# Kernel tuning notes

Measured on AMD Instinct MI355X. Metric: run time of the kernel, lower is better.

The kernel has to match this reference:

```python
import jax, jax.numpy as jnp
import numpy as np

N = 50000      # nodes
E = 640000     # edges
D = 128        # input/hidden dim
L = 3          # GIN layers
G = 256        # graphs in batch
LAT = 64       # latent dim
BN_EPS = 1e-5
SLOPE = 0.2    # LeakyReLU negative slope


def _leaky(h):
    return jnp.where(h >= 0, h, SLOPE * h)


def setup_inputs() -> dict:
    key = jax.random.key(0)
    ks = jax.random.split(key, 8)
    x = jax.random.normal(ks[0], (N, D), dtype=jnp.float32)
    edge_index = jax.random.randint(ks[1], (2, E), 0, N, dtype=jnp.int64)
    batch = jnp.sort(jax.random.randint(ks[2], (N,), 0, G, dtype=jnp.int64))
    W1 = jax.random.normal(ks[3], (L, D, D), dtype=jnp.float32) * 0.05
    W2 = jax.random.normal(ks[4], (L, D, D), dtype=jnp.float32) * 0.05
    fc_W = jax.random.normal(ks[5], (LAT, D), dtype=jnp.float32) * 0.05
    return {
        "x": x,
        "W1": W1,
        "b1": jnp.zeros((L, D), jnp.float32),
        "bn_g": jnp.ones((L, D), jnp.float32),
        "bn_b": jnp.zeros((L, D), jnp.float32),
        "bn_m": jnp.zeros((L, D), jnp.float32),
        "bn_v": jax.random.uniform(ks[6], (L, D), jnp.float32, 0.5, 1.5),
        "W2": W2,
        "b2": jnp.zeros((L, D), jnp.float32),
        "out_g": jnp.ones((D,), jnp.float32),
        "out_b": jnp.zeros((D,), jnp.float32),
        "out_m": jnp.zeros((D,), jnp.float32),
        "out_v": jax.random.uniform(ks[7], (D,), jnp.float32, 0.5, 1.5),
        "fc_W": fc_W,
        "fc_b": jnp.zeros((LAT,), jnp.float32),
        "edge_index": edge_index,
        "batch": batch,
    }


def reference(x, W1, b1, bn_g, bn_b, bn_m, bn_v, W2, b2,
              out_g, out_b, out_m, out_v, fc_W, fc_b,
              edge_index, batch):
    src, dst = edge_index[0], edge_index[1]
    for i in range(L):
        # GINConv: (1+eps)*x + sum_{j in N(i)} x_j  (eps=0 default)
        agg = x + jax.ops.segment_sum(x[src], dst, num_segments=N)
        # MLP: Linear -> LeakyReLU -> BatchNorm(eval) -> Linear -> LeakyReLU
        h = _leaky(agg @ W1[i].T + b1[i])
        h = (h - bn_m[i]) * jax.lax.rsqrt(bn_v[i] + BN_EPS) * bn_g[i] + bn_b[i]
        x = _leaky(h @ W2[i].T + b2[i])
        # dropout is identity in eval mode
    pooled = jax.ops.segment_sum(x, batch, num_segments=G)  # [G, D]
    out = (pooled - out_m) * jax.lax.rsqrt(out_v + BN_EPS) * out_g + out_b
    return out @ fc_W.T + fc_b  # [G, LAT]
```

## Files before the change

kernel.cpp:

```cpp
#include <hip/hip_runtime.h>
#include <cstdint>
#include <cstddef>

#define NN 50000
#define EE 640000
#define DD 128
#define LL 3
#define GG 256
#define LATD 64

typedef __attribute__((ext_vector_type(8))) __bf16 bf16x8;
typedef __attribute__((ext_vector_type(4))) float f32x4;

__device__ __forceinline__ unsigned short f2bf(float f) {
  __bf16 h = (__bf16)f;
  return __builtin_bit_cast(unsigned short, h);
}
__device__ __forceinline__ float bf2f(unsigned int u16) {
  unsigned int x = u16 << 16;
  return __builtin_bit_cast(float, x);
}
__device__ __forceinline__ void unpack8(uint4 v, float* f) {
  f[0] = bf2f(v.x & 0xffffu); f[1] = bf2f(v.x >> 16);
  f[2] = bf2f(v.y & 0xffffu); f[3] = bf2f(v.y >> 16);
  f[4] = bf2f(v.z & 0xffffu); f[5] = bf2f(v.z >> 16);
  f[6] = bf2f(v.w & 0xffffu); f[7] = bf2f(v.w >> 16);
}
__device__ __forceinline__ void acc8(uint4 v, float* f) {
  f[0] += bf2f(v.x & 0xffffu); f[1] += bf2f(v.x >> 16);
  f[2] += bf2f(v.y & 0xffffu); f[3] += bf2f(v.y >> 16);
  f[4] += bf2f(v.z & 0xffffu); f[5] += bf2f(v.z >> 16);
  f[6] += bf2f(v.w & 0xffffu); f[7] += bf2f(v.w >> 16);
}
__device__ __forceinline__ uint4 pack8(const float* f) {
  uint4 v;
  v.x = f2bf(f[0]) | ((unsigned)f2bf(f[1]) << 16);
  v.y = f2bf(f[2]) | ((unsigned)f2bf(f[3]) << 16);
  v.z = f2bf(f[4]) | ((unsigned)f2bf(f[5]) << 16);
  v.w = f2bf(f[6]) | ((unsigned)f2bf(f[7]) << 16);
  return v;
}

#define SWZ(byte_, row_) ((byte_) ^ (((row_) & 7) << 4))
#define CPAD 4

#define CVT_BLK 3125
#define WCV_BLK 48
#define HIST_BLK 2500
__global__ __launch_bounds__(256) void prep_kernel(
    const float4* __restrict__ x, uint4* __restrict__ xb,
    const float* __restrict__ W1, const float* __restrict__ W2,
    uint4* __restrict__ wb, const int* __restrict__ dst,
    int* __restrict__ counts) {
  int b = blockIdx.x;
  if (b < CVT_BLK) {
    int t = b * 256 + threadIdx.x;
    float4 a = x[t * 2], bb = x[t * 2 + 1];
    float f[8] = {a.x, a.y, a.z, a.w, bb.x, bb.y, bb.z, bb.w};
    xb[t] = pack8(f);
  } else if (b < CVT_BLK + WCV_BLK) {
    int t = (b - CVT_BLK) * 256 + threadIdx.x;
    int m = t >> 11;
    int q = t & 2047;
    int byte = q * 16;
    int row = byte >> 8;
    int inner = byte & 255;
    int isrc = inner ^ ((row & 7) << 4);
    int k0 = isrc >> 1;
    const float* Wsrc = (m & 1) ? W2 : W1;
    const float* p = Wsrc + ((size_t)(m >> 1) * DD * DD + row * DD + k0);
    float4 f0 = ((const float4*)p)[0], f1 = ((const float4*)p)[1];
    float f[8] = {f0.x, f0.y, f0.z, f0.w, f1.x, f1.y, f1.z, f1.w};
    wb[(size_t)m * 2048 + q] = pack8(f);
  } else {
    int e = (b - CVT_BLK - WCV_BLK) * 256 + threadIdx.x;
    atomicAdd(&counts[dst[e] << CPAD], 1);
  }
}

__global__ __launch_bounds__(256) void scan1_kernel(const int* __restrict__ counts,
                                                    int* __restrict__ rp,
                                                    int* __restrict__ bsum, int n) {
  int i = blockIdx.x * 256 + threadIdx.x;
  int v = (i < n) ? counts[i << CPAD] : 0;
  int lane = threadIdx.x & 63, w = threadIdx.x >> 6;
  int s = v;
#pragma unroll
  for (int off = 1; off < 64; off <<= 1) {
    int u = __shfl_up(s, off);
    if (lane >= off) s += u;
  }
  __shared__ int ws[4];
  if (lane == 63) ws[w] = s;
  __syncthreads();
  int add = 0;
#pragma unroll
  for (int k = 0; k < 4; ++k) if (k < w) add += ws[k];
  int incl = s + add;
  if (i < n) rp[i] = incl - v;
  if (threadIdx.x == 255) bsum[blockIdx.x] = incl;
}

__global__ __launch_bounds__(256) void scan2_kernel(int* __restrict__ bsum, int nb) {
  int t = threadIdx.x;
  int v = (t < nb) ? bsum[t] : 0;
  int lane = t & 63, w = t >> 6;
  int s = v;
#pragma unroll
  for (int off = 1; off < 64; off <<= 1) {
    int u = __shfl_up(s, off);
    if (lane >= off) s += u;
  }
  __shared__ int ws[4];
  if (lane == 63) ws[w] = s;
  __syncthreads();
  int add = 0;
#pragma unroll
  for (int k = 0; k < 4; ++k) if (k < w) add += ws[k];
  int incl = s + add;
  if (t < nb) bsum[t] = incl - v;
}

__global__ __launch_bounds__(256) void scan3_kernel(int* __restrict__ rp,
                                                    int* __restrict__ cursor,
                                                    const int* __restrict__ bsum, int n) {
  int i = blockIdx.x * 256 + threadIdx.x;
  if (i < n) {
    int v = rp[i] + bsum[blockIdx.x];
    rp[i] = v;
    cursor[i << CPAD] = v;
  }
  if (i == 0) rp[n] = EE;
}

__global__ __launch_bounds__(256) void fill_kernel(const int* __restrict__ src,
                                                   const int* __restrict__ dst,
                                                   int* __restrict__ cursor,
                                                   int* __restrict__ col, int E) {
  int e = blockIdx.x * blockDim.x + threadIdx.x;
  if (e < E) {
    int p = atomicAdd(&cursor[dst[e] << CPAD], 1);
    col[p] = src[e];
  }
}

__global__ __launch_bounds__(256, 4) void agg_kernel(const uint4* __restrict__ xin,
                                                     const int* __restrict__ row_ptr,
                                                     const int* __restrict__ colv,
                                                     uint4* __restrict__ agg, int n) {
  int tid = blockIdx.x * 256 + threadIdx.x;
  int node = tid >> 4;
  int c = tid & 15;
  if (node >= n) return;
  float acc[8];
  unpack8(xin[(size_t)node * 16 + c], acc);
  int s = row_ptr[node], e = row_ptr[node + 1];
  int j = s;
  for (; j + 8 <= e; j += 8) {
    int i0 = colv[j],     i1 = colv[j + 1], i2 = colv[j + 2], i3 = colv[j + 3];
    int i4 = colv[j + 4], i5 = colv[j + 5], i6 = colv[j + 6], i7 = colv[j + 7];
    uint4 v0 = xin[(size_t)i0 * 16 + c];
    uint4 v1 = xin[(size_t)i1 * 16 + c];
    uint4 v2 = xin[(size_t)i2 * 16 + c];
    uint4 v3 = xin[(size_t)i3 * 16 + c];
    uint4 v4 = xin[(size_t)i4 * 16 + c];
    uint4 v5 = xin[(size_t)i5 * 16 + c];
    uint4 v6 = xin[(size_t)i6 * 16 + c];
    uint4 v7 = xin[(size_t)i7 * 16 + c];
    acc8(v0, acc); acc8(v1, acc); acc8(v2, acc); acc8(v3, acc);
    acc8(v4, acc); acc8(v5, acc); acc8(v6, acc); acc8(v7, acc);
  }
  for (; j + 2 <= e; j += 2) {
    uint4 v0 = xin[(size_t)colv[j] * 16 + c];
    uint4 v1 = xin[(size_t)colv[j + 1] * 16 + c];
    acc8(v0, acc); acc8(v1, acc);
  }
  if (j < e) acc8(xin[(size_t)colv[j] * 16 + c], acc);
  agg[(size_t)node * 16 + c] = pack8(acc);
}

__global__ __launch_bounds__(512) void mlp128(
    const uint4* __restrict__ aggb, unsigned short* __restrict__ xout,
    const uint4* __restrict__ w1b, const uint4* __restrict__ w2b,
    const float* __restrict__ b1, const float* __restrict__ bng,
    const float* __restrict__ bnb, const float* __restrict__ bnm,
    const float* __restrict__ bnv, const float* __restrict__ b2, int n) {
  __shared__ __align__(16) char smem[98304];
  char* w1p = smem;
  char* w2p = smem + 32768;
  char* xp  = smem + 65536;

#pragma unroll
  for (int it = 0; it < 8; ++it) {
    int q = it * 512 + threadIdx.x;
    ((uint4*)w1p)[q] = w1b[q];
    ((uint4*)w2p)[q] = w2b[q];
  }

  int lane = threadIdx.x & 63;
  int c = lane & 15;
  int kq = lane >> 4;
  int wave = threadIdx.x >> 6;
  int r0 = wave * 16;

  float b1v[8], sv[8], tv[8], b2v[8];
#pragma unroll
  for (int ni = 0; ni < 8; ++ni) {
    int cc = ni * 16 + c;
    b1v[ni] = b1[cc];
    float s = bng[cc] * rsqrtf(bnv[cc] + 1e-5f);
    sv[ni] = s;
    tv[ni] = bnb[cc] - bnm[cc] * s;
    b2v[ni] = b2[cc];
  }

  for (int tile = blockIdx.x; tile * 128 < n; tile += 256) {
    int base = tile * 128;
#pragma unroll
    for (int it = 0; it < 4; ++it) {
      int t = it * 512 + threadIdx.x;
      int row = t >> 4, cc = t & 15;
      int grow = base + row;
      uint4 v = make_uint4(0, 0, 0, 0);
      if (grow < n) v = aggb[(size_t)grow * 16 + cc];
      *(uint4*)(xp + SWZ(row * 256 + cc * 16, row)) = v;
    }
    __syncthreads();

    f32x4 acc[8];
#pragma unroll
    for (int ni = 0; ni < 8; ++ni) acc[ni] = (f32x4){0.f, 0.f, 0.f, 0.f};

#pragma unroll
    for (int ks = 0; ks < 4; ++ks) {
      int row = r0 + c;
      bf16x8 a = *(const bf16x8*)(xp + SWZ(row * 256 + ks * 64 + kq * 16, row));
#pragma unroll
      for (int ni = 0; ni < 8; ++ni) {
        int wr = ni * 16 + c;
        bf16x8 bfr = *(const bf16x8*)(w1p + SWZ(wr * 256 + ks * 64 + kq * 16, wr));
        acc[ni] = __builtin_amdgcn_mfma_f32_16x16x32_bf16(a, bfr, acc[ni], 0, 0, 0);
      }
    }

#pragma unroll
    for (int ni = 0; ni < 8; ++ni)
#pragma unroll
      for (int r = 0; r < 4; ++r) {
        float h = acc[ni][r] + b1v[ni];
        h = h >= 0.f ? h : 0.2f * h;
        h = h * sv[ni] + tv[ni];
        int row = r0 + kq * 4 + r;
        *(__bf16*)(xp + SWZ(row * 256 + (ni * 16 + c) * 2, row)) = (__bf16)h;
      }
    __syncthreads();

#pragma unroll
    for (int ni = 0; ni < 8; ++ni) acc[ni] = (f32x4){0.f, 0.f, 0.f, 0.f};

#pragma unroll
    for (int ks = 0; ks < 4; ++ks) {
      int row = r0 + c;
      bf16x8 a = *(const bf16x8*)(xp + SWZ(row * 256 + ks * 64 + kq * 16, row));
#pragma unroll
      for (int ni = 0; ni < 8; ++ni) {
        int wr = ni * 16 + c;
        bf16x8 bfr = *(const bf16x8*)(w2p + SWZ(wr * 256 + ks * 64 + kq * 16, wr));
        acc[ni] = __builtin_amdgcn_mfma_f32_16x16x32_bf16(a, bfr, acc[ni], 0, 0, 0);
      }
    }

#pragma unroll
    for (int ni = 0; ni < 8; ++ni)
#pragma unroll
      for (int r = 0; r < 4; ++r) {
        float xo = acc[ni][r] + b2v[ni];
        xo = xo >= 0.f ? xo : 0.2f * xo;
        int grow = base + r0 + kq * 4 + r;
        if (grow < n) xout[(size_t)grow * DD + ni * 16 + c] = f2bf(xo);
      }
    __syncthreads();
  }
}

__global__ __launch_bounds__(256) void pool_kernel(const uint4* __restrict__ x,
                                                   const int* __restrict__ batch,
                                                   float* __restrict__ pooled, int n) {
  int gid = blockIdx.x * 256 + threadIdx.x;
  int grp = gid >> 4, c = gid & 15;
  int n0 = grp * 16;
  if (n0 >= n) return;
  float acc[8] = {0.f, 0.f, 0.f, 0.f, 0.f, 0.f, 0.f, 0.f};
  int curg = batch[n0];
  int end = n0 + 16 < n ? n0 + 16 : n;
  for (int node = n0; node < end; ++node) {
    int g = batch[node];
    if (g != curg) {
      float* p = pooled + (size_t)curg * DD + c * 8;
#pragma unroll
      for (int i = 0; i < 8; ++i) { atomicAdd(p + i, acc[i]); acc[i] = 0.f; }
      curg = g;
    }
    float tmp[8];
    unpack8(x[(size_t)node * 16 + c], tmp);
#pragma unroll
    for (int i = 0; i < 8; ++i) acc[i] += tmp[i];
  }
  float* p = pooled + (size_t)curg * DD + c * 8;
#pragma unroll
  for (int i = 0; i < 8; ++i) atomicAdd(p + i, acc[i]);
}

__global__ __launch_bounds__(128) void head_kernel(const float* __restrict__ pooled,
    const float* __restrict__ og, const float* __restrict__ ob,
    const float* __restrict__ om, const float* __restrict__ ov,
    const float* __restrict__ fcW, const float* __restrict__ fcb,
    float* __restrict__ out) {
  __shared__ float pb[DD];
  int g = blockIdx.x;
  int t = threadIdx.x;
  float s = og[t] * rsqrtf(ov[t] + 1e-5f);
  pb[t] = (pooled[(size_t)g * DD + t] - om[t]) * s + ob[t];
  __syncthreads();
  if (t < LATD) {
    float acc = fcb[t];
#pragma unroll 8
    for (int d = 0; d < DD; ++d) acc = fmaf(fcW[t * DD + d], pb[d], acc);
    out[(size_t)g * LATD + t] = acc;
  }
}

extern "C" void kernel_launch(void* const* d_in, const int* in_sizes, int n_in,
                              void* d_out, int out_size, void* d_ws, size_t ws_size,
                              hipStream_t stream) {
  const float* x   = (const float*)d_in[0];
  const float* W1  = (const float*)d_in[1];
  const float* b1  = (const float*)d_in[2];
  const float* bng = (const float*)d_in[3];
  const float* bnb = (const float*)d_in[4];
  const float* bnm = (const float*)d_in[5];
  const float* bnv = (const float*)d_in[6];
  const float* W2  = (const float*)d_in[7];
  const float* b2  = (const float*)d_in[8];
  const float* og  = (const float*)d_in[9];
  const float* ob  = (const float*)d_in[10];
  const float* om  = (const float*)d_in[11];
  const float* ov  = (const float*)d_in[12];
  const float* fcW = (const float*)d_in[13];
  const float* fcb = (const float*)d_in[14];
  const int* ei    = (const int*)d_in[15];
  const int* batch = (const int*)d_in[16];
  const int* src  = ei;
  const int* dstp = ei + EE;

  char* ws = (char*)d_ws;
  size_t off = 0;
  auto alloc = [&](size_t bytes) {
    void* p = ws + off;
    off += (bytes + 255) & ~(size_t)255;
    return p;
  };
  unsigned short* xb0  = (unsigned short*)alloc((size_t)NN * DD * 2);
  unsigned short* xb1  = (unsigned short*)alloc((size_t)NN * DD * 2);
  unsigned short* aggb = (unsigned short*)alloc((size_t)NN * DD * 2);
  uint4* wb     = (uint4*)alloc((size_t)6 * 2048 * 16);
  int* row_ptr  = (int*)alloc((NN + 1) * 4);
  int* cursor   = (int*)alloc((size_t)NN * 64);
  int* counts   = (int*)alloc((size_t)NN * 64);
  int* col      = (int*)alloc(EE * 4);
  int* bsum     = (int*)alloc(256 * 4);
  float* pooled = (float*)alloc(GG * DD * 4);

  hipMemsetAsync(counts, 0, (size_t)NN * 64, stream);
  hipMemsetAsync(pooled, 0, GG * DD * 4, stream);

  prep_kernel<<<CVT_BLK + WCV_BLK + HIST_BLK, 256, 0, stream>>>(
      (const float4*)x, (uint4*)xb0, W1, W2, wb, dstp, counts);

  const int NB = (NN + 255) / 256;
  scan1_kernel<<<NB, 256, 0, stream>>>(counts, row_ptr, bsum, NN);
  scan2_kernel<<<1, 256, 0, stream>>>(bsum, NB);
  scan3_kernel<<<NB, 256, 0, stream>>>(row_ptr, cursor, bsum, NN);
  fill_kernel<<<(EE + 255) / 256, 256, 0, stream>>>(src, dstp, cursor, col, EE);

  unsigned short* xcur = xb0;
  unsigned short* xnext = xb1;
  for (int i = 0; i < LL; ++i) {
    agg_kernel<<<(NN * 16 + 255) / 256, 256, 0, stream>>>(
        (const uint4*)xcur, row_ptr, col, (uint4*)aggb, NN);
    mlp128<<<256, 512, 0, stream>>>(
        (const uint4*)aggb, xnext,
        wb + (size_t)i * 4096, wb + (size_t)i * 4096 + 2048,
        b1 + i * DD, bng + i * DD, bnb + i * DD, bnm + i * DD, bnv + i * DD,
        b2 + i * DD, NN);
    unsigned short* t = xcur; xcur = xnext; xnext = t;
  }
  pool_kernel<<<(NN * 16 + 255) / 256, 256, 0, stream>>>(
      (const uint4*)xcur, batch, pooled, NN);
  head_kernel<<<GG, 128, 0, stream>>>(pooled, og, ob, om, ov, fcW, fcb, (float*)d_out);
}
```

Baseline: 232.0 us.

## Make MLP waves independent and fold pooling into head via sorted-batch search

The MLP kernel drops the block-wide tile staging and its __syncthreads barriers. Each wave now processes its own 16-row tile, reading A fragments straight from global memory and staging the hidden activations in a private shared-memory slice, then writes the output with coalesced 16-byte stores. The pool kernel, its atomics and the pooled buffer memset are removed. Instead, each head block binary-searches the sorted batch array for its node range and sums it directly. This relies on NN being divisible by 16 and on batch being sorted, and it makes the head kernel serial per graph, about 195 nodes each.

New measurement: 219.9 us, median of 2. -5.2%, faster.

```diff
diff --git a/kernel.cpp b/kernel.cpp
--- a/kernel.cpp
+++ b/kernel.cpp
@@ -179,29 +179,27 @@
   agg[(size_t)node * 16 + c] = pack8(acc);
 }
 
-__global__ __launch_bounds__(512) void mlp128(
-    const uint4* __restrict__ aggb, unsigned short* __restrict__ xout,
+__global__ __launch_bounds__(512) void mlp_nb(
+    const uint4* __restrict__ aggb, uint4* __restrict__ xout,
     const uint4* __restrict__ w1b, const uint4* __restrict__ w2b,
     const float* __restrict__ b1, const float* __restrict__ bng,
     const float* __restrict__ bnb, const float* __restrict__ bnm,
-    const float* __restrict__ bnv, const float* __restrict__ b2, int n) {
+    const float* __restrict__ bnv, const float* __restrict__ b2) {
   __shared__ __align__(16) char smem[98304];
   char* w1p = smem;
   char* w2p = smem + 32768;
-  char* xp  = smem + 65536;
-
 #pragma unroll
   for (int it = 0; it < 8; ++it) {
     int q = it * 512 + threadIdx.x;
     ((uint4*)w1p)[q] = w1b[q];
     ((uint4*)w2p)[q] = w2b[q];
   }
-
   int lane = threadIdx.x & 63;
   int c = lane & 15;
   int kq = lane >> 4;
   int wave = threadIdx.x >> 6;
-  int r0 = wave * 16;
+  char* hs = smem + 65536 + wave * 4096;
+  __syncthreads();
 
   float b1v[8], sv[8], tv[8], b2v[8];
 #pragma unroll
@@ -214,27 +212,15 @@
     b2v[ni] = b2[cc];
   }
 
-  for (int tile = blockIdx.x; tile * 128 < n; tile += 256) {
-    int base = tile * 128;
-#pragma unroll
-    for (int it = 0; it < 4; ++it) {
-      int t = it * 512 + threadIdx.x;
-      int row = t >> 4, cc = t & 15;
-      int grow = base + row;
-      uint4 v = make_uint4(0, 0, 0, 0);
-      if (grow < n) v = aggb[(size_t)grow * 16 + cc];
-      *(uint4*)(xp + SWZ(row * 256 + cc * 16, row)) = v;
-    }
-    __syncthreads();
-
+  for (int t = blockIdx.x * 8 + wave; t < NN / 16; t += 2048) {
+    int base = t * 16;
     f32x4 acc[8];
 #pragma unroll
     for (int ni = 0; ni < 8; ++ni) acc[ni] = (f32x4){0.f, 0.f, 0.f, 0.f};
 
 #pragma unroll
     for (int ks = 0; ks < 4; ++ks) {
-      int row = r0 + c;
-      bf16x8 a = *(const bf16x8*)(xp + SWZ(row * 256 + ks * 64 + kq * 16, row));
+      bf16x8 a = *(const bf16x8*)(aggb + (size_t)(base + c) * 16 + ks * 4 + kq);
 #pragma unroll
       for (int ni = 0; ni < 8; ++ni) {
         int wr = ni * 16 + c;
@@ -250,18 +236,16 @@
         float h = acc[ni][r] + b1v[ni];
         h = h >= 0.f ? h : 0.2f * h;
         h = h * sv[ni] + tv[ni];
-        int row = r0 + kq * 4 + r;
-        *(__bf16*)(xp + SWZ(row * 256 + (ni * 16 + c) * 2, row)) = (__bf16)h;
+        int row = kq * 4 + r;
+        *(__bf16*)(hs + row * 256 + SWZ((ni * 16 + c) * 2, row)) = (__bf16)h;
       }
-    __syncthreads();
 
 #pragma unroll
     for (int ni = 0; ni < 8; ++ni) acc[ni] = (f32x4){0.f, 0.f, 0.f, 0.f};
 
 #pragma unroll
     for (int ks = 0; ks < 4; ++ks) {
-      int row = r0 + c;
-      bf16x8 a = *(const bf16x8*)(xp + SWZ(row * 256 + ks * 64 + kq * 16, row));
+      bf16x8 a = *(const bf16x8*)(hs + c * 256 + SWZ(ks * 64 + kq * 16, c));
 #pragma unroll
       for (int ni = 0; ni < 8; ++ni) {
         int wr = ni * 16 + c;
@@ -276,57 +260,55 @@
       for (int r = 0; r < 4; ++r) {
         float xo = acc[ni][r] + b2v[ni];
         xo = xo >= 0.f ? xo : 0.2f * xo;
-        int grow = base + r0 + kq * 4 + r;
-        if (grow < n) xout[(size_t)grow * DD + ni * 16 + c] = f2bf(xo);
+        int row = kq * 4 + r;
+        *(__bf16*)(hs + row * 256 + (ni * 16 + c) * 2) = (__bf16)xo;
       }
-    __syncthreads();
-  }
-}
-
-__global__ __launch_bounds__(256) void pool_kernel(const uint4* __restrict__ x,
-                                                   const int* __restrict__ batch,
-                                                   float* __restrict__ pooled, int n) {
-  int gid = blockIdx.x * 256 + threadIdx.x;
-  int grp = gid >> 4, c = gid & 15;
-  int n0 = grp * 16;
-  if (n0 >= n) return;
-  float acc[8] = {0.f, 0.f, 0.f, 0.f, 0.f, 0.f, 0.f, 0.f};
-  int curg = batch[n0];
-  int end = n0 + 16 < n ? n0 + 16 : n;
-  for (int node = n0; node < end; ++node) {
-    int g = batch[node];
-    if (g != curg) {
-      float* p = pooled + (size_t)curg * DD + c * 8;
-#pragma unroll
-      for (int i = 0; i < 8; ++i) { atomicAdd(p + i, acc[i]); acc[i] = 0.f; }
-      curg = g;
+#pragma unroll
+    for (int it2 = 0; it2 < 4; ++it2) {
+      int chunk = it2 * 64 + lane;
+      uint4 v = *(const uint4*)(hs + chunk * 16);
+      xout[(size_t)base * 16 + chunk] = v;
     }
-    float tmp[8];
-    unpack8(x[(size_t)node * 16 + c], tmp);
-#pragma unroll
-    for (int i = 0; i < 8; ++i) acc[i] += tmp[i];
-  }
-  float* p = pooled + (size_t)curg * DD + c * 8;
-#pragma unroll
-  for (int i = 0; i < 8; ++i) atomicAdd(p + i, acc[i]);
-}
-
-__global__ __launch_bounds__(128) void head_kernel(const float* __restrict__ pooled,
+  }
+}
+
+__global__ __launch_bounds__(128) void head_kernel(
+    const unsigned short* __restrict__ x, const int* __restrict__ batch,
     const float* __restrict__ og, const float* __restrict__ ob,
     const float* __restrict__ om, const float* __restrict__ ov,
     const float* __restrict__ fcW, const float* __restrict__ fcb,
     float* __restrict__ out) {
   __shared__ float pb[DD];
+  __shared__ int slo, shi;
   int g = blockIdx.x;
   int t = threadIdx.x;
+  if (t == 0) {
+    int lo = 0, hi = NN;
+    while (lo < hi) { int m = (lo + hi) >> 1; if (batch[m] < g) lo = m + 1; else hi = m; }
+    slo = lo;
+    lo = 0; hi = NN;
+    while (lo < hi) { int m = (lo + hi) >> 1; if (batch[m] < g + 1) lo = m + 1; else hi = m; }
+    shi = lo;
+  }
+  __syncthreads();
+  float acc = 0.f;
+  int node = slo;
+  for (; node + 4 <= shi; node += 4) {
+    float a0 = bf2f(x[(size_t)(node + 0) * DD + t]);
+    float a1 = bf2f(x[(size_t)(node + 1) * DD + t]);
+    float a2 = bf2f(x[(size_t)(node + 2) * DD + t]);
+    float a3 = bf2f(x[(size_t)(node + 3) * DD + t]);
+    acc += (a0 + a1) + (a2 + a3);
+  }
+  for (; node < shi; ++node) acc += bf2f(x[(size_t)node * DD + t]);
   float s = og[t] * rsqrtf(ov[t] + 1e-5f);
-  pb[t] = (pooled[(size_t)g * DD + t] - om[t]) * s + ob[t];
+  pb[t] = (acc - om[t]) * s + ob[t];
   __syncthreads();
   if (t < LATD) {
-    float acc = fcb[t];
+    float a = fcb[t];
 #pragma unroll 8
-    for (int d = 0; d < DD; ++d) acc = fmaf(fcW[t * DD + d], pb[d], acc);
-    out[(size_t)g * LATD + t] = acc;
+    for (int d = 0; d < DD; ++d) a = fmaf(fcW[t * DD + d], pb[d], a);
+    out[(size_t)g * LATD + t] = a;
   }
 }
 
@@ -369,10 +351,8 @@
   int* counts   = (int*)alloc((size_t)NN * 64);
   int* col      = (int*)alloc(EE * 4);
   int* bsum     = (int*)alloc(256 * 4);
-  float* pooled = (float*)alloc(GG * DD * 4);
 
   hipMemsetAsync(counts, 0, (size_t)NN * 64, stream);
-  hipMemsetAsync(pooled, 0, GG * DD * 4, stream);
 
   prep_kernel<<<CVT_BLK + WCV_BLK + HIST_BLK, 256, 0, stream>>>(
       (const float4*)x, (uint4*)xb0, W1, W2, wb, dstp, counts);
@@ -388,14 +368,13 @@
   for (int i = 0; i < LL; ++i) {
     agg_kernel<<<(NN * 16 + 255) / 256, 256, 0, stream>>>(
         (const uint4*)xcur, row_ptr, col, (uint4*)aggb, NN);
-    mlp128<<<256, 512, 0, stream>>>(
-        (const uint4*)aggb, xnext,
+    mlp_nb<<<256, 512, 0, stream>>>(
+        (const uint4*)aggb, (uint4*)xnext,
         wb + (size_t)i * 4096, wb + (size_t)i * 4096 + 2048,
         b1 + i * DD, bng + i * DD, bnb + i * DD, bnm + i * DD, bnv + i * DD,
-        b2 + i * DD, NN);
+        b2 + i * DD);
     unsigned short* t = xcur; xcur = xnext; xnext = t;
   }
-  pool_kernel<<<(NN * 16 + 255) / 256, 256, 0, stream>>>(
-      (const uint4*)xcur, batch, pooled, NN);
-  head_kernel<<<GG, 128, 0, stream>>>(pooled, og, ob, om, ov, fcW, fcb, (float*)d_out);
-}
+  head_kernel<<<GG, 128, 0, stream>>>(
+      xcur, batch, og, ob, om, ov, fcW, fcb, (float*)d_out);
+}
```
